# Performance work log

Measured on AMD Instinct MI355X. Metric: run time of the kernel, lower is better.

The kernel has to match this reference:

```python
import jax, jax.numpy as jnp
import numpy as np

B, S, H = 32, 4096, 1024


def setup_inputs() -> dict:
    key = jax.random.key(0)
    k1, k2, k3, k4 = jax.random.split(key, 4)
    hidden = jax.random.normal(k1, (B, 1, H), dtype=jnp.float32)
    encoder_outputs = jax.random.normal(k2, (B, S, H), dtype=jnp.float32)
    # nn.Linear(H, H): weight [H, H], bias [H]; scaled like torch default-ish init
    W = jax.random.normal(k3, (H, H), dtype=jnp.float32) / np.sqrt(H)
    b = jax.random.normal(k4, (H,), dtype=jnp.float32) / np.sqrt(H)
    return {"hidden": hidden, "encoder_outputs": encoder_outputs, "W": W, "b": b}


def reference(hidden, encoder_outputs, W, b):
    # method == 'general': energy_i = Linear(enc_i); score_i = hidden[:,0] . energy_i
    energy = jnp.einsum('bsh,kh->bsk', encoder_outputs, W) + b  # [B,S,H]
    attn_energies = jnp.einsum('bh,bsh->bs', hidden[:, 0], energy)  # [B,S]
    return jax.nn.softmax(attn_energies, axis=1)
```

## Files before the change

### kernel.cpp

```cpp
#include <hip/hip_runtime.h>
#include <math.h>

#define BB 32
#define SS 4096
#define HH 1024

typedef float fvec4 __attribute__((ext_vector_type(4)));

__global__ __launch_bounds__(256) void compute_v_kernel(
        const float* __restrict__ hidden,
        const float* __restrict__ W,
        float* __restrict__ v) {
    const int b = blockIdx.y;
    const int h = blockIdx.x * 256 + threadIdx.x;
    const int k0 = blockIdx.z * 128;
    const float* __restrict__ hb = hidden + b * HH + k0;
    const float* __restrict__ Wp = W + (size_t)k0 * HH + h;
    float acc = 0.f;
#pragma unroll 8
    for (int k = 0; k < 128; ++k)
        acc = fmaf(hb[k], Wp[(size_t)k * HH], acc);
    atomicAdd(&v[b * HH + h], acc);
}

__global__ __launch_bounds__(256) void compute_scores_kernel(
        const float* __restrict__ enc,
        const float* __restrict__ v,
        float* __restrict__ scores) {
    const int b = blockIdx.y;
    const int wave = threadIdx.x >> 6;
    const int lane = threadIdx.x & 63;
    const int s0 = (blockIdx.x * 4 + wave) * 4;

    const fvec4* __restrict__ v4 = (const fvec4*)(v + b * HH);
    const fvec4 w0 = v4[lane];
    const fvec4 w1 = v4[64 + lane];
    const fvec4 w2 = v4[128 + lane];
    const fvec4 w3 = v4[192 + lane];

    const fvec4* __restrict__ e4 =
        (const fvec4*)(enc + ((size_t)b * SS + s0) * HH);

    float acc[4];
#pragma unroll
    for (int j = 0; j < 4; ++j) {
        const fvec4* __restrict__ p = e4 + (size_t)j * 256;
        fvec4 e0 = p[lane];
        fvec4 e1 = p[64 + lane];
        fvec4 e2 = p[128 + lane];
        fvec4 e3 = p[192 + lane];
        fvec4 t = e0 * w0 + e1 * w1 + e2 * w2 + e3 * w3;
        acc[j] = t.x + t.y + t.z + t.w;
    }
#pragma unroll
    for (int j = 0; j < 4; ++j) {
#pragma unroll
        for (int off = 32; off > 0; off >>= 1)
            acc[j] += __shfl_xor(acc[j], off, 64);
    }
    if (lane == 0) {
        fvec4 r = {acc[0], acc[1], acc[2], acc[3]};
        *(fvec4*)(scores + (size_t)b * SS + s0) = r;
    }
}

__global__ __launch_bounds__(1024) void softmax_kernel(float* __restrict__ scores) {
    const int b = blockIdx.x;
    float* __restrict__ row = scores + (size_t)b * SS;
    const int tid = threadIdx.x;
    const int lane = tid & 63;
    const int wave = tid >> 6;

    __shared__ float red_max[16];
    __shared__ float red_sum[16];

    float vals[4];
    float m = -INFINITY;
#pragma unroll
    for (int i = 0; i < 4; ++i) {
        vals[i] = row[i * 1024 + tid];
        m = fmaxf(m, vals[i]);
    }
#pragma unroll
    for (int off = 32; off > 0; off >>= 1)
        m = fmaxf(m, __shfl_xor(m, off, 64));
    if (lane == 0) red_max[wave] = m;
    __syncthreads();
#pragma unroll
    for (int i = 0; i < 16; ++i) m = fmaxf(m, red_max[i]);

    float sum = 0.f;
#pragma unroll
    for (int i = 0; i < 4; ++i) {
        vals[i] = __expf(vals[i] - m);
        sum += vals[i];
    }
#pragma unroll
    for (int off = 32; off > 0; off >>= 1)
        sum += __shfl_xor(sum, off, 64);
    if (lane == 0) red_sum[wave] = sum;
    __syncthreads();
    sum = 0.f;
#pragma unroll
    for (int i = 0; i < 16; ++i) sum += red_sum[i];

    const float inv = 1.f / sum;
#pragma unroll
    for (int i = 0; i < 4; ++i)
        row[i * 1024 + tid] = vals[i] * inv;
}

extern "C" void kernel_launch(void* const* d_in, const int* in_sizes, int n_in,
                              void* d_out, int out_size, void* d_ws, size_t ws_size,
                              hipStream_t stream) {
    const float* hidden = (const float*)d_in[0];
    const float* enc    = (const float*)d_in[1];
    const float* W      = (const float*)d_in[2];
    float* out = (float*)d_out;
    float* v   = (float*)d_ws;

    hipMemsetAsync(v, 0, (size_t)BB * HH * sizeof(float), stream);
    compute_v_kernel<<<dim3(HH / 256, BB, 8), 256, 0, stream>>>(hidden, W, v);
    compute_scores_kernel<<<dim3(SS / 16, BB), 256, 0, stream>>>(enc, v, out);
    softmax_kernel<<<BB, 1024, 0, stream>>>(out);
}
```

Before: 689.4 us.

## Compute one score per thread with shared v, remove atomics in v kernel

The v projection now reduces its K-slices within a block through shared memory, replacing the global atomicAdd and the memset. The scores kernel assigns one sequence row per thread and caches v in LDS, replacing the wave-cooperative dot product with a shuffle reduction. The aim is to remove the shuffle reductions and the launch overhead. The risk is that per-thread row reads are strided by 4 KB across lanes, which breaks coalescing on the dominant encoder read.

```diff
diff --git a/kernel.cpp b/kernel.cpp
--- a/kernel.cpp
+++ b/kernel.cpp
@@ -12,15 +12,26 @@
         const float* __restrict__ W,
         float* __restrict__ v) {
     const int b = blockIdx.y;
-    const int h = blockIdx.x * 256 + threadIdx.x;
-    const int k0 = blockIdx.z * 128;
+    const int hl = threadIdx.x & 63;
+    const int h = blockIdx.x * 64 + hl;
+    const int slice = threadIdx.x >> 6;
+    const int k0 = slice * 256;
     const float* __restrict__ hb = hidden + b * HH + k0;
     const float* __restrict__ Wp = W + (size_t)k0 * HH + h;
-    float acc = 0.f;
+    float a0 = 0.f, a1 = 0.f, a2 = 0.f, a3 = 0.f;
 #pragma unroll 8
-    for (int k = 0; k < 128; ++k)
-        acc = fmaf(hb[k], Wp[(size_t)k * HH], acc);
-    atomicAdd(&v[b * HH + h], acc);
+    for (int k = 0; k < 256; k += 4) {
+        a0 = fmaf(hb[k + 0], Wp[(size_t)(k + 0) * HH], a0);
+        a1 = fmaf(hb[k + 1], Wp[(size_t)(k + 1) * HH], a1);
+        a2 = fmaf(hb[k + 2], Wp[(size_t)(k + 2) * HH], a2);
+        a3 = fmaf(hb[k + 3], Wp[(size_t)(k + 3) * HH], a3);
+    }
+    __shared__ float red[256];
+    red[threadIdx.x] = (a0 + a1) + (a2 + a3);
+    __syncthreads();
+    if (threadIdx.x < 64)
+        v[b * HH + h] =
+            (red[hl] + red[64 + hl]) + (red[128 + hl] + red[192 + hl]);
 }
 
 __global__ __launch_bounds__(256) void compute_scores_kernel(
@@ -28,40 +39,32 @@
         const float* __restrict__ v,
         float* __restrict__ scores) {
     const int b = blockIdx.y;
-    const int wave = threadIdx.x >> 6;
-    const int lane = threadIdx.x & 63;
-    const int s0 = (blockIdx.x * 4 + wave) * 4;
+    const int s = blockIdx.x * 256 + threadIdx.x;
 
-    const fvec4* __restrict__ v4 = (const fvec4*)(v + b * HH);
-    const fvec4 w0 = v4[lane];
-    const fvec4 w1 = v4[64 + lane];
-    const fvec4 w2 = v4[128 + lane];
-    const fvec4 w3 = v4[192 + lane];
+    __shared__ fvec4 vs[HH / 4];
+    vs[threadIdx.x] = ((const fvec4*)(v + (size_t)b * HH))[threadIdx.x];
+    __syncthreads();
 
-    const fvec4* __restrict__ e4 =
-        (const fvec4*)(enc + ((size_t)b * SS + s0) * HH);
+    const fvec4* __restrict__ e =
+        (const fvec4*)(enc + ((size_t)b * SS + s) * HH);
 
-    float acc[4];
-#pragma unroll
-    for (int j = 0; j < 4; ++j) {
-        const fvec4* __restrict__ p = e4 + (size_t)j * 256;
-        fvec4 e0 = p[lane];
-        fvec4 e1 = p[64 + lane];
-        fvec4 e2 = p[128 + lane];
-        fvec4 e3 = p[192 + lane];
-        fvec4 t = e0 * w0 + e1 * w1 + e2 * w2 + e3 * w3;
-        acc[j] = t.x + t.y + t.z + t.w;
+    fvec4 acc0 = {0.f, 0.f, 0.f, 0.f};
+    fvec4 acc1 = {0.f, 0.f, 0.f, 0.f};
+#pragma unroll 2
+    for (int k = 0; k < HH / 4; k += 8) {
+        fvec4 e0 = e[k + 0], e1 = e[k + 1], e2 = e[k + 2], e3 = e[k + 3];
+        fvec4 e4 = e[k + 4], e5 = e[k + 5], e6 = e[k + 6], e7 = e[k + 7];
+        acc0 += e0 * vs[k + 0];
+        acc1 += e1 * vs[k + 1];
+        acc0 += e2 * vs[k + 2];
+        acc1 += e3 * vs[k + 3];
+        acc0 += e4 * vs[k + 4];
+        acc1 += e5 * vs[k + 5];
+        acc0 += e6 * vs[k + 6];
+        acc1 += e7 * vs[k + 7];
     }
-#pragma unroll
-    for (int j = 0; j < 4; ++j) {
-#pragma unroll
-        for (int off = 32; off > 0; off >>= 1)
-            acc[j] += __shfl_xor(acc[j], off, 64);
-    }
-    if (lane == 0) {
-        fvec4 r = {acc[0], acc[1], acc[2], acc[3]};
-        *(fvec4*)(scores + (size_t)b * SS + s0) = r;
-    }
+    const fvec4 t = acc0 + acc1;
+    scores[(size_t)b * SS + s] = (t.x + t.y) + (t.z + t.w);
 }
 
 __global__ __launch_bounds__(1024) void softmax_kernel(float* __restrict__ scores) {
@@ -119,8 +122,7 @@
     float* out = (float*)d_out;
     float* v   = (float*)d_ws;
 
-    hipMemsetAsync(v, 0, (size_t)BB * HH * sizeof(float), stream);
-    compute_v_kernel<<<dim3(HH / 256, BB, 8), 256, 0, stream>>>(hidden, W, v);
-    compute_scores_kernel<<<dim3(SS / 16, BB), 256, 0, stream>>>(enc, v, out);
+    compute_v_kernel<<<dim3(HH / 64, BB), 256, 0, stream>>>(hidden, W, v);
+    compute_scores_kernel<<<dim3(SS / 256, BB), 256, 0, stream>>>(enc, v, out);
     softmax_kernel<<<BB, 1024, 0, stream>>>(out);
 }
```

New measurement: 734.5 us. +6.6%, slower.

## Drop atomics and memset in v projection, use nontemporal enc loads

Applied to the files above, without the earlier changes.

The v = hidden·W kernel now splits K across the four waves of a block and reduces them through shared memory, so it no longer needs atomicAdd or the memset launch before it. The scores kernel reads the encoder stream with nontemporal loads and replaces four separate 64-lane butterfly reductions with a combined transpose-style shuffle reduction. Lanes 0-3 write the scores as scalars instead of one lane writing a vector. These changes aim to cut launch overhead and atomic traffic and to reduce cache pollution from the large enc stream. The dominant cost is still streaming 512MB of enc, so gains are likely small.

```diff
diff --git a/kernel.cpp b/kernel.cpp
--- a/kernel.cpp
+++ b/kernel.cpp
@@ -12,15 +12,26 @@
         const float* __restrict__ W,
         float* __restrict__ v) {
     const int b = blockIdx.y;
-    const int h = blockIdx.x * 256 + threadIdx.x;
-    const int k0 = blockIdx.z * 128;
+    const int hl = threadIdx.x & 63;
+    const int h = blockIdx.x * 64 + hl;
+    const int slice = threadIdx.x >> 6;
+    const int k0 = slice * 256;
     const float* __restrict__ hb = hidden + b * HH + k0;
     const float* __restrict__ Wp = W + (size_t)k0 * HH + h;
-    float acc = 0.f;
+    float a0 = 0.f, a1 = 0.f, a2 = 0.f, a3 = 0.f;
 #pragma unroll 8
-    for (int k = 0; k < 128; ++k)
-        acc = fmaf(hb[k], Wp[(size_t)k * HH], acc);
-    atomicAdd(&v[b * HH + h], acc);
+    for (int k = 0; k < 256; k += 4) {
+        a0 = fmaf(hb[k + 0], Wp[(size_t)(k + 0) * HH], a0);
+        a1 = fmaf(hb[k + 1], Wp[(size_t)(k + 1) * HH], a1);
+        a2 = fmaf(hb[k + 2], Wp[(size_t)(k + 2) * HH], a2);
+        a3 = fmaf(hb[k + 3], Wp[(size_t)(k + 3) * HH], a3);
+    }
+    __shared__ float red[256];
+    red[threadIdx.x] = (a0 + a1) + (a2 + a3);
+    __syncthreads();
+    if (threadIdx.x < 64)
+        v[b * HH + h] =
+            (red[hl] + red[64 + hl]) + (red[128 + hl] + red[192 + hl]);
 }
 
 __global__ __launch_bounds__(256) void compute_scores_kernel(
@@ -45,23 +56,30 @@
 #pragma unroll
     for (int j = 0; j < 4; ++j) {
         const fvec4* __restrict__ p = e4 + (size_t)j * 256;
-        fvec4 e0 = p[lane];
-        fvec4 e1 = p[64 + lane];
-        fvec4 e2 = p[128 + lane];
-        fvec4 e3 = p[192 + lane];
+        fvec4 e0 = __builtin_nontemporal_load(&p[lane]);
+        fvec4 e1 = __builtin_nontemporal_load(&p[64 + lane]);
+        fvec4 e2 = __builtin_nontemporal_load(&p[128 + lane]);
+        fvec4 e3 = __builtin_nontemporal_load(&p[192 + lane]);
         fvec4 t = e0 * w0 + e1 * w1 + e2 * w2 + e3 * w3;
         acc[j] = t.x + t.y + t.z + t.w;
     }
-#pragma unroll
-    for (int j = 0; j < 4; ++j) {
-#pragma unroll
-        for (int off = 32; off > 0; off >>= 1)
-            acc[j] += __shfl_xor(acc[j], off, 64);
-    }
-    if (lane == 0) {
-        fvec4 r = {acc[0], acc[1], acc[2], acc[3]};
-        *(fvec4*)(scores + (size_t)b * SS + s0) = r;
-    }
+
+    float t0 = acc[0] + __shfl_xor(acc[0], 1, 64);
+    float t1 = acc[1] + __shfl_xor(acc[1], 1, 64);
+    float t2 = acc[2] + __shfl_xor(acc[2], 1, 64);
+    float t3 = acc[3] + __shfl_xor(acc[3], 1, 64);
+    float r01 = (lane & 1) ? t1 : t0;
+    float r23 = (lane & 1) ? t3 : t2;
+    float u01 = r01 + __shfl_xor(r01, 2, 64);
+    float u23 = r23 + __shfl_xor(r23, 2, 64);
+    float r = (lane & 2) ? u23 : u01;
+    r += __shfl_xor(r, 4, 64);
+    r += __shfl_xor(r, 8, 64);
+    r += __shfl_xor(r, 16, 64);
+    r += __shfl_xor(r, 32, 64);
+
+    if (lane < 4)
+        scores[(size_t)b * SS + s0 + lane] = r;
 }
 
 __global__ __launch_bounds__(1024) void softmax_kernel(float* __restrict__ scores) {
@@ -119,8 +137,7 @@
     float* out = (float*)d_out;
     float* v   = (float*)d_ws;
 
-    hipMemsetAsync(v, 0, (size_t)BB * HH * sizeof(float), stream);
-    compute_v_kernel<<<dim3(HH / 256, BB, 8), 256, 0, stream>>>(hidden, W, v);
+    compute_v_kernel<<<dim3(HH / 64, BB), 256, 0, stream>>>(hidden, W, v);
     compute_scores_kernel<<<dim3(SS / 16, BB), 256, 0, stream>>>(enc, v, out);
     softmax_kernel<<<BB, 1024, 0, stream>>>(out);
 }
```

After: 672.0 us. 1.03x faster.
